# Kernel tuning notes

Hardware: AMD Instinct MI355X
Metric: run time of the kernel (lower is better)

## Reference

```python
import jax, jax.numpy as jnp
import numpy as np

# Model dims
C = 16          # in_channels / d_model
D_INNER = 64    # expand * C, expand = 64 // C = 4
HEADDIM = 4
NHEADS = D_INNER // HEADDIM   # 16
D_STATE = 64
D_CONV = 4
CONV_DIM = D_INNER + 2 * D_STATE        # 192 (x, B, C streams)
D_IN_PROJ = 2 * D_INNER + 2 * D_STATE + NHEADS  # 272 (z, xBC, dt)
# Input volume
BSZ, DD, HH, WW = 8, 32, 16, 16
L = DD * HH * WW  # 8192, multiple of 256 -> exact adaptive max pool
POOL = 256


def setup_inputs():
    key = jax.random.key(0)
    ks = jax.random.split(key, 10)
    x = jax.random.normal(ks[0], (BSZ, C, DD, HH, WW), jnp.float32)
    # 3 independent Mamba2 blocks -> stack params with leading dim 3
    Win = jax.random.normal(ks[1], (3, D_IN_PROJ, C), jnp.float32) / np.sqrt(C).astype(np.float32)
    conv_w = jax.random.normal(ks[2], (3, CONV_DIM, D_CONV), jnp.float32) / np.sqrt(D_CONV).astype(np.float32)
    conv_b = jax.random.normal(ks[3], (3, CONV_DIM), jnp.float32) * 0.1
    dt_bias = jax.random.normal(ks[4], (3, NHEADS), jnp.float32) * 0.5
    A_log = jnp.log(jax.random.uniform(ks[5], (3, NHEADS), jnp.float32, minval=1.0, maxval=16.0))
    Dp = jax.random.normal(ks[6], (3, NHEADS), jnp.float32) * 0.5 + 1.0
    norm_w = jnp.ones((3, D_INNER), jnp.float32)
    Wout = jax.random.normal(ks[7], (3, C, D_INNER), jnp.float32) / np.sqrt(D_INNER).astype(np.float32)
    gamma = jnp.ones((3, C), jnp.float32)
    beta = jnp.zeros((3, C), jnp.float32)
    lin_w = jax.random.normal(ks[8], (3, 1, C), jnp.float32) / np.sqrt(C).astype(np.float32)
    lin_b = jnp.zeros((3, 1), jnp.float32)
    return dict(x=x, Win=Win, conv_w=conv_w, conv_b=conv_b, dt_bias=dt_bias,
                A_log=A_log, Dp=Dp, norm_w=norm_w, Wout=Wout,
                gamma=gamma, beta=beta, lin_w=lin_w, lin_b=lin_b)


def _mamba2(u, Win, conv_w, conv_b, dt_bias, A_log, Dp, norm_w, Wout):
    """Mamba2 block: u (B, L, C) -> (B, L, C). ngroups=1, rmsnorm gated."""
    B, Lx, _ = u.shape
    zxbcdt = jnp.einsum('blc,pc->blp', u, Win)  # (B, L, 272)
    z = zxbcdt[..., :D_INNER]
    xBC = zxbcdt[..., D_INNER:D_INNER + CONV_DIM]
    dt = jax.nn.softplus(zxbcdt[..., D_INNER + CONV_DIM:] + dt_bias)  # (B, L, H)
    # causal depthwise conv over time
    conv = jax.lax.conv_general_dilated(
        jnp.transpose(xBC, (0, 2, 1)), conv_w[:, None, :], (1,),
        [(D_CONV - 1, 0)], feature_group_count=CONV_DIM)
    xBC = jax.nn.silu(jnp.transpose(conv, (0, 2, 1)) + conv_b)
    xh = xBC[..., :D_INNER].reshape(B, Lx, NHEADS, HEADDIM)
    Bm = xBC[..., D_INNER:D_INNER + D_STATE]   # (B, L, N)
    Cm = xBC[..., D_INNER + D_STATE:]          # (B, L, N)
    A = -jnp.exp(A_log)                        # (H,)
    dA = jnp.exp(dt * A)                       # (B, L, H)
    dtx = dt[..., None] * xh                   # (B, L, H, P)

    def step(S, inp):
        dA_t, dtx_t, B_t, C_t = inp
        S = S * dA_t[:, :, None, None] + dtx_t[..., None] * B_t[:, None, None, :]
        y_t = jnp.einsum('bhpn,bn->bhp', S, C_t)
        return S, y_t

    S0 = jnp.zeros((B, NHEADS, HEADDIM, D_STATE), u.dtype)
    xs = (jnp.moveaxis(dA, 1, 0), jnp.moveaxis(dtx, 1, 0),
          jnp.moveaxis(Bm, 1, 0), jnp.moveaxis(Cm, 1, 0))
    _, ys = jax.lax.scan(step, S0, xs)                       # (L, B, H, P)
    y = jnp.moveaxis(ys, 0, 1) + Dp[None, None, :, None] * xh
    y = y.reshape(B, Lx, D_INNER) * jax.nn.silu(z)           # gate first
    y = y * jax.lax.rsqrt(jnp.mean(y * y, -1, keepdims=True) + 1e-5) * norm_w
    return jnp.einsum('bld,cd->blc', y, Wout)


def _proj_pool(y, gamma, beta, lw, lb):
    """ReLU -> BatchNorm1d (batch stats) -> Linear(C,1) -> AdaptiveMaxPool1d(256)."""
    B, Lx, _ = y.shape
    v = jax.nn.relu(y.reshape(-1, C))
    mu = jnp.mean(v, 0)
    var = jnp.mean((v - mu) ** 2, 0)
    v = (v - mu) * jax.lax.rsqrt(var + 1e-5) * gamma + beta
    s = (v @ lw.T + lb).reshape(B, Lx)
    return jnp.max(s.reshape(B, POOL, Lx // POOL), -1)  # (B, 256)


def reference(x, Win, conv_w, conv_b, dt_bias, A_log, Dp, norm_w, Wout,
              gamma, beta, lin_w, lin_b):
    B, Cc, Dd, Hh, Ww = x.shape
    Lx = Dd * Hh * Ww
    fD = jnp.transpose(x.reshape(B, Cc, Lx), (0, 2, 1))
    fH = jnp.transpose(jnp.transpose(x, (0, 1, 3, 4, 2)).reshape(B, Cc, Lx), (0, 2, 1))
    fW = jnp.transpose(jnp.transpose(x, (0, 1, 4, 2, 3)).reshape(B, Cc, Lx), (0, 2, 1))
    seqs = jnp.stack([fD, fH, fW], 0)  # (3, B, L, C)
    ys = jax.vmap(_mamba2)(seqs, Win, conv_w, conv_b, dt_bias, A_log, Dp, norm_w, Wout)
    pooled = jax.vmap(_proj_pool)(ys, gamma, beta, lin_w, lin_b)  # (3, B, 256)
    return jnp.concatenate([pooled[0], pooled[1], pooled[2]], -1)[:, None, :]  # (B,1,768)
```

## Files before the change

kernel.cpp:

```cpp
#include <hip/hip_runtime.h>
#include <math.h>

#define CONVD 192
#define NC 128
#define PW 32
#define LOG2E 1.4426950408889634f
#define LN2f  0.69314718055994531f

#define OFF_DST   0u
#define OFF_CHA   4194304u
#define OFF_YS    4210688u
#define OFF_PART  5259264u
#define OFF_TILE  5267456u
#define PD        19947520u

#define TXH 0
#define TC  4096
#define TG  8192
#define TDT 12288
#define TCT 13312

#define XSW(m, t)   ((m) * 64 + (((((t) >> 2) ^ ((m) & 15)) & 15) << 2) + ((t) & 3))
#define XSW4(m, tq) ((m) * 64 + ((((tq) ^ ((m) & 15)) & 15) << 2))

typedef float f32x2 __attribute__((ext_vector_type(2)));

__device__ __forceinline__ f32x2 pk_fma(f32x2 a, f32x2 b, f32x2 c) {
    f32x2 d;
    asm("v_pk_fma_f32 %0, %1, %2, %3" : "=v"(d) : "v"(a), "v"(b), "v"(c));
    return d;
}
__device__ __forceinline__ f32x2 lo2(float4 v) { f32x2 r; r.x = v.x; r.y = v.y; return r; }
__device__ __forceinline__ f32x2 hi2(float4 v) { f32x2 r; r.x = v.z; r.y = v.w; return r; }

__device__ __forceinline__ float fast_silu(float x) {
    float e = __builtin_amdgcn_exp2f(-x * LOG2E);
    return x * __builtin_amdgcn_rcpf(1.f + e);
}
__device__ __forceinline__ float fast_softplus(float x) {
    if (x > 20.f) return x;
    float e = __builtin_amdgcn_exp2f(x * LOG2E);
    return LN2f * __builtin_amdgcn_logf(1.f + e);
}

template<int NT>
__device__ __forceinline__ void stage_u(
    const float* __restrict__ x, float* u_s, int b, int l0, int dir, int tid)
{
    for (int i = tid; i < 67 * 16; i += NT) {
        int pos = i >> 4, c = i & 15;
        int l = l0 + pos - 3;
        float v = 0.f;
        if (l >= 0) {
            if (dir == 0) {
                v = x[(b * 16 + c) * 8192 + l];
            } else if (dir == 1) {
                int h = l >> 9, w = (l >> 5) & 15, d = l & 31;
                v = x[(((b * 16 + c) * 32 + d) * 16 + h) * 16 + w];
            } else {
                int w = l >> 9, d = (l >> 4) & 31, h = l & 15;
                v = x[(((b * 16 + c) * 32 + d) * 16 + h) * 16 + w];
            }
        }
        u_s[pos * 17 + c] = v;
    }
}

__device__ __forceinline__ float pk_dot16(const f32x2* u2, const float* wp) {
    float4 w0 = *(const float4*)(wp);
    float4 w1 = *(const float4*)(wp + 4);
    float4 w2 = *(const float4*)(wp + 8);
    float4 w3 = *(const float4*)(wp + 12);
    f32x2 a = {0.f, 0.f};
    a = pk_fma(u2[0], lo2(w0), a);
    a = pk_fma(u2[1], hi2(w0), a);
    a = pk_fma(u2[2], lo2(w1), a);
    a = pk_fma(u2[3], hi2(w1), a);
    a = pk_fma(u2[4], lo2(w2), a);
    a = pk_fma(u2[5], hi2(w2), a);
    a = pk_fma(u2[6], lo2(w3), a);
    a = pk_fma(u2[7], hi2(w3), a);
    return a.x + a.y;
}

__global__ __launch_bounds__(512, 6) void k_front(
    const float* __restrict__ x, const float* __restrict__ Win,
    const float* __restrict__ convw, const float* __restrict__ convb,
    const float* __restrict__ dtb, const float* __restrict__ A_log,
    float* __restrict__ ws, int dir0, int dslm)
{
    __shared__ float u_s[67 * 17];
    __shared__ float xh_c[4096];
    __shared__ float Bs[4096];
    __shared__ float dts[16 * 65];
    __shared__ float wbuf[16 * 65];
    const int tid = threadIdx.x;
    const int ck = blockIdx.x;
    const int b = blockIdx.y;
    const int dir = dir0 + blockIdx.z;
    float* base = ws + (size_t)(dslm * blockIdx.z) * PD;
    float* Dst = base + OFF_DST;
    float* chA = base + OFF_CHA;
    float* tile = base + OFF_TILE + (size_t)(b * 128 + ck) * 14336;
    const int l0 = ck * 64;
    float* halo = wbuf;

    stage_u<512>(x, u_s, b, l0, dir, tid);
    __syncthreads();

    const int lane = tid & 63;
    const int wv = __builtin_amdgcn_readfirstlane(tid >> 6);

    f32x2 u2[8];
    {
        const float* ur = &u_s[(lane + 3) * 17];
        #pragma unroll
        for (int k = 0; k < 8; k++) { u2[k].x = ur[2 * k]; u2[k].y = ur[2 * k + 1]; }
    }
    if (tid < 192) {
        f32x2 uh2[8];
        #pragma unroll
        for (int pos = 0; pos < 3; pos++) {
            const float* uhr = &u_s[pos * 17];
            #pragma unroll
            for (int k = 0; k < 8; k++) { uh2[k].x = uhr[2 * k]; uh2[k].y = uhr[2 * k + 1]; }
            halo[pos * 192 + tid] = pk_dot16(uh2, Win + (size_t)(dir * 272 + 64 + tid) * 16);
        }
    }
    __syncthreads();

    for (int i = 0; i < 26; i++) {
        const int col = 64 + wv * 26 + i;
        float acc = pk_dot16(u2, Win + (size_t)(dir * 272 + col) * 16);
        if (col < 256) {
            const int ch = col - 64;
            float v1 = __shfl_up(acc, 1);
            float v2 = __shfl_up(acc, 2);
            float v3 = __shfl_up(acc, 3);
            float hh0 = halo[ch];
            float hh1 = halo[192 + ch];
            float hh2 = halo[384 + ch];
            float m1 = (lane >= 1) ? v1 : hh2;
            float m2 = (lane >= 2) ? v2 : ((lane == 0) ? hh1 : hh2);
            float m3 = (lane >= 3) ? v3 : ((lane == 0) ? hh0 : ((lane == 1) ? hh1 : hh2));
            const float* cwp = convw + (size_t)(dir * CONVD + ch) * 4;
            float conv = convb[dir * CONVD + ch]
                       + cwp[0] * m3 + cwp[1] * m2 + cwp[2] * m1 + cwp[3] * acc;
            float xv = fast_silu(conv);
            if (ch < 64)       xh_c[XSW(ch, lane)] = xv;
            else if (ch < 128) Bs[XSW(ch - 64, lane)] = xv;
            else               tile[TC + (ch - 128) * 64 + lane] = xv;
        } else {
            const int h = col - 256;
            float dv = fast_softplus(acc + dtb[dir * 16 + h]);
            dts[h * 65 + lane] = dv;
            tile[TDT + h * 64 + lane] = dv;
        }
    }
    __syncthreads();

    for (int j4 = tid; j4 < 1024; j4 += 512) {
        ((float4*)(tile + TXH))[j4] = ((const float4*)xh_c)[j4];
    }
    for (int h = wv; h < 16; h += 8) {
        float A2 = -expf(A_log[dir * 16 + h]) * LOG2E;
        float dtv = dts[h * 65 + lane];
        float v = dtv * A2;
        #pragma unroll
        for (int off = 1; off < 64; off <<= 1) {
            float o = __shfl_up(v, off, 64);
            if (lane >= off) v += o;
        }
        float tot = __shfl(v, 63, 64);
        tile[TCT + h * 64 + lane] = v;
        wbuf[h * 65 + lane] = __builtin_amdgcn_exp2f(tot - v) * dtv;
        if (lane == 63) chA[(b * 16 + h) * 128 + ck] = __builtin_amdgcn_exp2f(tot);
    }
    __syncthreads();

    for (int j = tid; j < 4096; j += 512) {
        int hp = j >> 6, t = j & 63;
        xh_c[XSW(hp, t)] *= wbuf[(hp >> 2) * 65 + t];
    }
    __syncthreads();

    if (tid < 256) {
        const int hp4 = tid >> 4, n4 = tid & 15;
        f32x2 a2[4][4] = {};
        for (int tq = 0; tq < 16; tq++) {
            float4 xv[4], bv[4];
            #pragma unroll
            for (int i2 = 0; i2 < 4; i2++) {
                xv[i2] = *(const float4*)&xh_c[XSW4(4 * hp4 + i2, tq)];
                bv[i2] = *(const float4*)&Bs[XSW4(4 * n4 + i2, tq)];
            }
            #pragma unroll
            for (int i2 = 0; i2 < 4; i2++)
                #pragma unroll
                for (int j2 = 0; j2 < 4; j2++) {
                    a2[i2][j2] = pk_fma(lo2(xv[i2]), lo2(bv[j2]), a2[i2][j2]);
                    a2[i2][j2] = pk_fma(hi2(xv[i2]), hi2(bv[j2]), a2[i2][j2]);
                }
        }
        #pragma unroll
        for (int i2 = 0; i2 < 4; i2++) {
            int hp = 4 * hp4 + i2;
            int h = hp >> 2, p = hp & 3;
            *(float4*)(Dst + ((size_t)((b * 16 + h) * 128 + ck)) * 256 + p * 64 + 4 * n4) =
                make_float4(a2[i2][0].x + a2[i2][0].y, a2[i2][1].x + a2[i2][1].y,
                            a2[i2][2].x + a2[i2][2].y, a2[i2][3].x + a2[i2][3].y);
        }
    } else {
        const int tg2 = tid - 256;
        const int t4g = tg2 >> 4, x4g = tg2 & 15;
        float G_[4][4] = {};
        for (int n = 0; n < 64; n++) {
            float4 cr4 = *(const float4*)(tile + TC + n * 64 + 4 * t4g);
            float4 br4 = *(const float4*)&Bs[XSW4(n, x4g)];
            float cr[4] = {cr4.x, cr4.y, cr4.z, cr4.w};
            float br_[4] = {br4.x, br4.y, br4.z, br4.w};
            #pragma unroll
            for (int r = 0; r < 4; r++)
                #pragma unroll
                for (int q = 0; q < 4; q++)
                    G_[r][q] += cr[r] * br_[q];
        }
        float* gdst = tile + TG + (size_t)tg2 * 16;
        #pragma unroll
        for (int r = 0; r < 4; r++)
            *(float4*)(gdst + 4 * r) = make_float4(G_[r][0], G_[r][1], G_[r][2], G_[r][3]);
    }
}

__global__ __launch_bounds__(64) void k_chunk_scan(
    float* __restrict__ ws, int dslm)
{
    float* base = ws + (size_t)(dslm * blockIdx.z) * PD;
    float* Dst = base + OFF_DST;
    const float* chA = base + OFF_CHA;
    const int bh = blockIdx.x >> 2;
    const int elem = (blockIdx.x & 3) * 64 + threadIdx.x;
    float S = 0.f;
    for (int k0 = 0; k0 < NC; k0 += 8) {
        float d[8], av[8];
        #pragma unroll
        for (int j = 0; j < 8; j++) {
            d[j] = Dst[((size_t)(bh * 128 + k0 + j)) * 256 + elem];
            av[j] = chA[bh * 128 + k0 + j];
        }
        #pragma unroll
        for (int j = 0; j < 8; j++) {
            Dst[((size_t)(bh * 128 + k0 + j)) * 256 + elem] = S;
            S = av[j] * S + d[j];
        }
    }
}

__global__ __launch_bounds__(512, 2) void k_out_epi(
    const float* __restrict__ x, const float* __restrict__ Win,
    const float* __restrict__ Dp, const float* __restrict__ normw,
    const float* __restrict__ Wout, float* __restrict__ ws, int dir0, int dslm)
{
    __shared__ float SinT[64 * 68];
    __shared__ float xh_c[4096];
    __shared__ float Bz[4096];
    __shared__ float Cy[4352];
    __shared__ float uW[67 * 17];
    __shared__ float dts[16 * 68];
    __shared__ float ct2l[16 * 68];
    __shared__ float Dps[16];
    float* base = ws + (size_t)(dslm * blockIdx.z) * PD;
    const float* Dst = base + OFF_DST;
    float* ys        = base + OFF_YS;
    float* partials  = base + OFF_PART;
    const float* tile = base + OFF_TILE + (size_t)(blockIdx.y * 128 + blockIdx.x) * 14336;
    const int dir = dir0 + blockIdx.z;
    const int tid = threadIdx.x;
    const int b = blockIdx.y;
    const int ck = blockIdx.x;
    const int l0 = ck * 64;
    const int tg = tid & 255;
    const int t4 = tg >> 4, x4 = tg & 15;
    const int grp = tid >> 8;
    const int lane = tid & 63;
    const int wv = __builtin_amdgcn_readfirstlane(tid >> 6);

    stage_u<512>(x, uW, b, l0, dir, tid);
    for (int j4 = tid; j4 < 1024; j4 += 512) {
        ((float4*)xh_c)[j4] = ((const float4*)(tile + TXH))[j4];
        ((float4*)Cy)[j4]   = ((const float4*)(tile + TC))[j4];
    }
    if (tid < 256) {
        int h = tid >> 4, tq = tid & 15;
        *(float4*)&dts[h * 68 + 4 * tq]  = ((const float4*)(tile + TDT))[tid];
        *(float4*)&ct2l[h * 68 + 4 * tq] = ((const float4*)(tile + TCT))[tid];
    }
    for (int j = tid; j < 1024; j += 512) {
        int hp = j >> 4, n4 = (j & 15) << 2;
        int h = hp >> 2, p = hp & 3;
        float4 sv = *(const float4*)(Dst + ((size_t)((b * 16 + h) * 128 + ck)) * 256 + p * 64 + n4);
        SinT[(n4 + 0) * 68 + hp] = sv.x;
        SinT[(n4 + 1) * 68 + hp] = sv.y;
        SinT[(n4 + 2) * 68 + hp] = sv.z;
        SinT[(n4 + 3) * 68 + hp] = sv.w;
    }
    float G_[4][4];
    {
        const float* gsrc = tile + TG + (size_t)tg * 16;
        #pragma unroll
        for (int r = 0; r < 4; r++) {
            float4 g4 = *(const float4*)(gsrc + 4 * r);
            G_[r][0] = g4.x; G_[r][1] = g4.y; G_[r][2] = g4.z; G_[r][3] = g4.w;
        }
    }
    if (tid < 16) Dps[tid] = Dp[dir * 16 + tid];
    __syncthreads();

    {
        f32x2 u2[8];
        const float* ur = &uW[(lane + 3) * 17];
        #pragma unroll
        for (int k = 0; k < 8; k++) { u2[k].x = ur[2 * k]; u2[k].y = ur[2 * k + 1]; }
        for (int i = 0; i < 8; i++) {
            const int col = wv * 8 + i;
            Bz[XSW(col, lane)] = pk_dot16(u2, Win + (size_t)(dir * 272 + col) * 16);
        }
    }
    float CS_[4][4] = {};
    {
        const int n0 = grp << 5;
        for (int n = n0; n < n0 + 32; n++) {
            float4 cr4 = *(const float4*)&Cy[n * 64 + 4 * t4];
            float cr[4] = {cr4.x, cr4.y, cr4.z, cr4.w};
            float sn[4];
            #pragma unroll
            for (int q = 0; q < 4; q++) sn[q] = SinT[n * 68 + 4 * x4 + q];
            #pragma unroll
            for (int r = 0; r < 4; r++)
                #pragma unroll
                for (int q = 0; q < 4; q++)
                    CS_[r][q] += cr[r] * sn[q];
        }
    }
    __syncthreads();

    {
        float* ex = (grp == 0) ? SinT : Cy;
        #pragma unroll
        for (int k = 0; k < 16; k++) ex[tg * 17 + k] = CS_[k >> 2][k & 3];
    }
    for (int j = tid; j < 1024; j += 512) {
        int c = j >> 6, d = j & 63;
        uW[c * 65 + d] = Wout[dir * 1024 + j] * normw[dir * 64 + d];
    }
    __syncthreads();
    {
        const float* ex = (grp == 0) ? Cy : SinT;
        #pragma unroll
        for (int k = 0; k < 16; k++) CS_[k >> 2][k & 3] += ex[tg * 17 + k];
    }
    __syncthreads();

    float* yv = Cy;
    const int tbase = 4 * t4;
    #pragma unroll 1
    for (int hh = 0; hh < 8; hh++) {
        const int h = 8 * grp + hh;
        const float* ctp = &ct2l[h * 68];
        const float* dtp = &dts[h * 68];
        float4 ctt4 = *(const float4*)&ctp[tbase];
        const float ctt[4] = {ctt4.x, ctt4.y, ctt4.z, ctt4.w};
        float ect[4];
        #pragma unroll
        for (int r = 0; r < 4; r++) ect[r] = __builtin_amdgcn_exp2f(ctt[r]);
        float4 cs4 = *(const float4*)&ctp[4 * x4];
        float4 dt4 = *(const float4*)&dtp[4 * x4];
        float v[16] = {0.f, 0.f, 0.f, 0.f, 0.f, 0.f, 0.f, 0.f,
                       0.f, 0.f, 0.f, 0.f, 0.f, 0.f, 0.f, 0.f};
        #pragma unroll
        for (int q = 0; q < 4; q++) {
            const int s = 4 * x4 + q;
            float csq = (q == 0) ? cs4.x : (q == 1) ? cs4.y : (q == 2) ? cs4.z : cs4.w;
            float dtq = (q == 0) ? dt4.x : (q == 1) ? dt4.y : (q == 2) ? dt4.z : dt4.w;
            float xv[4];
            #pragma unroll
            for (int p = 0; p < 4; p++) {
                int m = 4 * h + p;
                xv[p] = xh_c[m * 64 + (((x4 ^ (m & 15)) & 15) << 2) + q];
            }
            #pragma unroll
            for (int r = 0; r < 4; r++) {
                float e = __builtin_amdgcn_exp2f(ctt[r] - csq);
                float w = (s <= tbase + r) ? (G_[r][q] * dtq) * e : 0.f;
                #pragma unroll
                for (int p = 0; p < 4; p++) v[4 * r + p] += w * xv[p];
            }
        }
        if (x4 == h) {
            #pragma unroll
            for (int r = 0; r < 4; r++)
                #pragma unroll
                for (int p = 0; p < 4; p++)
                    v[4 * r + p] += ect[r] * CS_[r][p];
        }
        #pragma unroll
        for (int j = 0; j < 8; j++) {
            float a = (x4 & 8) ? v[j + 8] : v[j];
            float s_ = (x4 & 8) ? v[j] : v[j + 8];
            v[j] = a + __shfl_xor(s_, 8);
        }
        #pragma unroll
        for (int j = 0; j < 4; j++) {
            float a = (x4 & 4) ? v[j + 4] : v[j];
            float s_ = (x4 & 4) ? v[j] : v[j + 4];
            v[j] = a + __shfl_xor(s_, 4);
        }
        #pragma unroll
        for (int j = 0; j < 2; j++) {
            float a = (x4 & 2) ? v[j + 2] : v[j];
            float s_ = (x4 & 2) ? v[j] : v[j + 2];
            v[j] = a + __shfl_xor(s_, 2);
        }
        {
            float a = (x4 & 1) ? v[1] : v[0];
            float s_ = (x4 & 1) ? v[0] : v[1];
            v[0] = a + __shfl_xor(s_, 1);
        }
        const int row = tbase + (x4 >> 2);
        yv[(row * 4 + (x4 & 3)) * 17 + h] = v[0];
    }
    __syncthreads();

    float* red = ct2l;
    float os[4];
    const int row = tid >> 2;
    const int p = tid & 3;
    if (tid < 256) {
        float gg[16], sumsq = 0.f;
        #pragma unroll
        for (int h = 0; h < 16; h++) {
            float yval = yv[(row * 4 + p) * 17 + h];
            int m = 4 * h + p;
            int ax = m * 64 + ((((row >> 2) ^ (m & 15)) & 15) << 2) + (row & 3);
            float xh = xh_c[ax];
            float zv = Bz[ax];
            float val = (yval + Dps[h] * xh) * fast_silu(zv);
            gg[h] = val;
            sumsq += val * val;
        }
        sumsq += __shfl_xor(sumsq, 1);
        sumsq += __shfl_xor(sumsq, 2);
        float rms = rsqrtf(sumsq * (1.f / 64.f) + 1e-5f);

        float oc[16];
        #pragma unroll
        for (int c = 0; c < 16; c++) {
            float a = 0.f;
            #pragma unroll
            for (int h = 0; h < 16; h++) a += gg[h] * uW[c * 65 + 4 * h + p];
            oc[c] = a;
        }
        #pragma unroll
        for (int c = 0; c < 16; c++) {
            oc[c] += __shfl_xor(oc[c], 1);
            oc[c] += __shfl_xor(oc[c], 2);
        }
        #pragma unroll
        for (int i2 = 0; i2 < 4; i2++) {
            float a0 = (p == 0) ? oc[i2] : oc[4 + i2];
            float a1 = (p == 2) ? oc[8 + i2] : oc[12 + i2];
            os[i2] = (((p & 2) == 0) ? a0 : a1) * rms;
        }
        size_t bl = (size_t)(b * 8192 + l0 + row);
        *(float4*)(ys + bl * 16 + 4 * p) = make_float4(os[0], os[1], os[2], os[3]);

        float bs[4], bq[4];
        #pragma unroll
        for (int i2 = 0; i2 < 4; i2++) {
            float vv = fmaxf(os[i2], 0.f);
            bs[i2] = vv;
            bq[i2] = vv * vv;
        }
        #pragma unroll
        for (int off = 4; off < 64; off <<= 1) {
            #pragma unroll
            for (int i2 = 0; i2 < 4; i2++) {
                bs[i2] += __shfl_xor(bs[i2], off);
                bq[i2] += __shfl_xor(bq[i2], off);
            }
        }
        const int wlane = tid & 63, wvid = tid >> 6;
        if (wlane < 4) {
            #pragma unroll
            for (int i2 = 0; i2 < 4; i2++) {
                red[wvid * 34 + 4 * wlane + i2] = bs[i2];
                red[wvid * 34 + 16 + 4 * wlane + i2] = bq[i2];
            }
        }
    }
    __syncthreads();
    if (tid < 32) {
        float a = red[0 * 34 + tid] + red[1 * 34 + tid]
                + red[2 * 34 + tid] + red[3 * 34 + tid];
        partials[((size_t)(b * 128 + ck)) * 32 + tid] = a;
    }
}

__global__ __launch_bounds__(256) void k_pool_bn(
    const float* __restrict__ gamma, const float* __restrict__ beta,
    const float* __restrict__ lin_w, const float* __restrict__ lin_b,
    float* __restrict__ ws, float* __restrict__ out, int dir0, int dslm)
{
    float* base = ws + (size_t)(dslm * blockIdx.z) * PD;
    const float* ys = base + OFF_YS;
    const float* partials = base + OFF_PART;
    const int dir = dir0 + blockIdx.z;
    const int tid = threadIdx.x;
    __shared__ float red[8][33];
    __shared__ float cf[18];
    {
        int c = tid & 31, ks = tid >> 5;
        float a = 0.f;
        for (int k = ks * 128; k < ks * 128 + 128; k++) a += partials[k * 32 + c];
        red[ks][c] = a;
    }
    __syncthreads();
    if (tid < 32) {
        float a = 0.f;
        #pragma unroll
        for (int s2 = 1; s2 < 8; s2++) a += red[s2][tid];
        red[0][tid] += a;
    }
    __syncthreads();
    if (tid == 0) {
        float off = lin_b[dir];
        for (int c = 0; c < 16; c++) {
            float mu = red[0][c] * (1.f / 65536.f);
            float var = red[0][16 + c] * (1.f / 65536.f) - mu * mu;
            float inv = rsqrtf(var + 1e-5f);
            float coef = inv * gamma[dir * 16 + c] * lin_w[dir * 16 + c];
            cf[c] = coef;
            off += beta[dir * 16 + c] * lin_w[dir * 16 + c] - mu * coef;
        }
        cf[16] = off;
    }
    __syncthreads();

    const int b = blockIdx.x >> 3;
    const int jg = blockIdx.x & 7;
    const int j = jg * 32 + (tid >> 3);
    const int sub = tid & 7;
    float m = -3.4e38f;
    #pragma unroll
    for (int r = 0; r < 4; r++) {
        int l = j * PW + 8 * r + sub;
        const float* rowp = ys + (size_t)(b * 8192 + l) * 16;
        float sv = cf[16];
        #pragma unroll
        for (int k = 0; k < 4; k++) {
            float4 v4 = *(const float4*)(rowp + 4 * k);
            sv += fmaxf(v4.x, 0.f) * cf[4 * k] + fmaxf(v4.y, 0.f) * cf[4 * k + 1]
                + fmaxf(v4.z, 0.f) * cf[4 * k + 2] + fmaxf(v4.w, 0.f) * cf[4 * k + 3];
        }
        m = fmaxf(m, sv);
    }
    m = fmaxf(m, __shfl_xor(m, 1));
    m = fmaxf(m, __shfl_xor(m, 2));
    m = fmaxf(m, __shfl_xor(m, 4));
    if (sub == 0) out[b * 768 + dir * 256 + j] = m;
}

extern "C" void kernel_launch(void* const* d_in, const int* in_sizes, int n_in,
                              void* d_out, int out_size, void* d_ws, size_t ws_size,
                              hipStream_t stream) {
    const float* x     = (const float*)d_in[0];
    const float* Win   = (const float*)d_in[1];
    const float* convw = (const float*)d_in[2];
    const float* convb = (const float*)d_in[3];
    const float* dtb   = (const float*)d_in[4];
    const float* Alog  = (const float*)d_in[5];
    const float* Dp    = (const float*)d_in[6];
    const float* normw = (const float*)d_in[7];
    const float* Wout  = (const float*)d_in[8];
    const float* gamma = (const float*)d_in[9];
    const float* beta  = (const float*)d_in[10];
    const float* linw  = (const float*)d_in[11];
    const float* linb  = (const float*)d_in[12];
    float* out = (float*)d_out;
    float* ws = (float*)d_ws;

    const bool batched = ws_size >= (size_t)3 * PD * 4;
    const int nz = batched ? 3 : 1;
    const int dslm = batched ? 1 : 0;
    const int nloop = batched ? 1 : 3;

    for (int d0 = 0; d0 < nloop; ++d0) {
        k_front<<<dim3(128, 8, nz), dim3(512), 0, stream>>>(
            x, Win, convw, convb, dtb, Alog, ws, d0, dslm);
        k_chunk_scan<<<dim3(512, 1, nz), dim3(64), 0, stream>>>(ws, dslm);
        k_out_epi<<<dim3(128, 8, nz), dim3(512), 0, stream>>>(
            x, Win, Dp, normw, Wout, ws, d0, dslm);
        k_pool_bn<<<dim3(64, 1, nz), dim3(256), 0, stream>>>(
            gamma, beta, linw, linb, ws, out, d0, dslm);
    }
}
```

Measured before the change: 368.3 us.

## Recompute x and C streams in output kernel instead of round-tripping workspace

k_front no longer writes the post-conv x and C tiles to the global workspace. k_out_epi now recomputes the in-projection, the causal conv with its halo, and SiLU for the x and C channels from the staged input. This shrinks the per-chunk tile and the overall workspace, removing a large global write and read between kernels. The cost is extra projection and conv arithmetic plus more barriers in k_out_epi. k_front also gains a shared C buffer, and its launch-bounds occupancy hint drops from 6 to 4. Some leftover dead code remains in the new halo setup.

```diff
diff --git a/kernel.cpp b/kernel.cpp
--- a/kernel.cpp
+++ b/kernel.cpp
@@ -12,13 +12,11 @@
 #define OFF_YS    4210688u
 #define OFF_PART  5259264u
 #define OFF_TILE  5267456u
-#define PD        19947520u
-
-#define TXH 0
-#define TC  4096
-#define TG  8192
-#define TDT 12288
-#define TCT 13312
+#define PD        11558912u
+
+#define TG  0
+#define TDT 4096
+#define TCT 5120
 
 #define XSW(m, t)   ((m) * 64 + (((((t) >> 2) ^ ((m) & 15)) & 15) << 2) + ((t) & 3))
 #define XSW4(m, tq) ((m) * 64 + ((((tq) ^ ((m) & 15)) & 15) << 2))
@@ -83,7 +81,7 @@
     return a.x + a.y;
 }
 
-__global__ __launch_bounds__(512, 6) void k_front(
+__global__ __launch_bounds__(512, 4) void k_front(
     const float* __restrict__ x, const float* __restrict__ Win,
     const float* __restrict__ convw, const float* __restrict__ convb,
     const float* __restrict__ dtb, const float* __restrict__ A_log,
@@ -92,6 +90,7 @@
     __shared__ float u_s[67 * 17];
     __shared__ float xh_c[4096];
     __shared__ float Bs[4096];
+    __shared__ float Cc[4096];
     __shared__ float dts[16 * 65];
     __shared__ float wbuf[16 * 65];
     const int tid = threadIdx.x;
@@ -101,7 +100,7 @@
     float* base = ws + (size_t)(dslm * blockIdx.z) * PD;
     float* Dst = base + OFF_DST;
     float* chA = base + OFF_CHA;
-    float* tile = base + OFF_TILE + (size_t)(b * 128 + ck) * 14336;
+    float* tile = base + OFF_TILE + (size_t)(b * 128 + ck) * 6144;
     const int l0 = ck * 64;
     float* halo = wbuf;
 
@@ -149,7 +148,7 @@
             float xv = fast_silu(conv);
             if (ch < 64)       xh_c[XSW(ch, lane)] = xv;
             else if (ch < 128) Bs[XSW(ch - 64, lane)] = xv;
-            else               tile[TC + (ch - 128) * 64 + lane] = xv;
+            else               Cc[XSW(ch - 128, lane)] = xv;
         } else {
             const int h = col - 256;
             float dv = fast_softplus(acc + dtb[dir * 16 + h]);
@@ -159,9 +158,6 @@
     }
     __syncthreads();
 
-    for (int j4 = tid; j4 < 1024; j4 += 512) {
-        ((float4*)(tile + TXH))[j4] = ((const float4*)xh_c)[j4];
-    }
     for (int h = wv; h < 16; h += 8) {
         float A2 = -expf(A_log[dir * 16 + h]) * LOG2E;
         float dtv = dts[h * 65 + lane];
@@ -215,7 +211,7 @@
         const int t4g = tg2 >> 4, x4g = tg2 & 15;
         float G_[4][4] = {};
         for (int n = 0; n < 64; n++) {
-            float4 cr4 = *(const float4*)(tile + TC + n * 64 + 4 * t4g);
+            float4 cr4 = *(const float4*)&Cc[XSW4(n, t4g)];
             float4 br4 = *(const float4*)&Bs[XSW4(n, x4g)];
             float cr[4] = {cr4.x, cr4.y, cr4.z, cr4.w};
             float br_[4] = {br4.x, br4.y, br4.z, br4.w};
@@ -258,6 +254,7 @@
 
 __global__ __launch_bounds__(512, 2) void k_out_epi(
     const float* __restrict__ x, const float* __restrict__ Win,
+    const float* __restrict__ convw, const float* __restrict__ convb,
     const float* __restrict__ Dp, const float* __restrict__ normw,
     const float* __restrict__ Wout, float* __restrict__ ws, int dir0, int dslm)
 {
@@ -273,7 +270,7 @@
     const float* Dst = base + OFF_DST;
     float* ys        = base + OFF_YS;
     float* partials  = base + OFF_PART;
-    const float* tile = base + OFF_TILE + (size_t)(blockIdx.y * 128 + blockIdx.x) * 14336;
+    const float* tile = base + OFF_TILE + (size_t)(blockIdx.y * 128 + blockIdx.x) * 6144;
     const int dir = dir0 + blockIdx.z;
     const int tid = threadIdx.x;
     const int b = blockIdx.y;
@@ -286,10 +283,6 @@
     const int wv = __builtin_amdgcn_readfirstlane(tid >> 6);
 
     stage_u<512>(x, uW, b, l0, dir, tid);
-    for (int j4 = tid; j4 < 1024; j4 += 512) {
-        ((float4*)xh_c)[j4] = ((const float4*)(tile + TXH))[j4];
-        ((float4*)Cy)[j4]   = ((const float4*)(tile + TC))[j4];
-    }
     if (tid < 256) {
         int h = tid >> 4, tq = tid & 15;
         *(float4*)&dts[h * 68 + 4 * tq]  = ((const float4*)(tile + TDT))[tid];
@@ -304,33 +297,82 @@
         SinT[(n4 + 2) * 68 + hp] = sv.z;
         SinT[(n4 + 3) * 68 + hp] = sv.w;
     }
-    float G_[4][4];
+    if (tid < 16) Dps[tid] = Dp[dir * 16 + tid];
+    __syncthreads();
+
+    f32x2 u2[8];
     {
-        const float* gsrc = tile + TG + (size_t)tg * 16;
-        #pragma unroll
-        for (int r = 0; r < 4; r++) {
-            float4 g4 = *(const float4*)(gsrc + 4 * r);
-            G_[r][0] = g4.x; G_[r][1] = g4.y; G_[r][2] = g4.z; G_[r][3] = g4.w;
-        }
-    }
-    if (tid < 16) Dps[tid] = Dp[dir * 16 + tid];
-    __syncthreads();
-
-    {
-        f32x2 u2[8];
         const float* ur = &uW[(lane + 3) * 17];
         #pragma unroll
         for (int k = 0; k < 8; k++) { u2[k].x = ur[2 * k]; u2[k].y = ur[2 * k + 1]; }
-        for (int i = 0; i < 8; i++) {
-            const int col = wv * 8 + i;
-            Bz[XSW(col, lane)] = pk_dot16(u2, Win + (size_t)(dir * 272 + col) * 16);
-        }
-    }
+    }
+    f32x2 uh2[8];
+    if (tid < 192) {
+        #pragma unroll
+        for (int k = 0; k < 8; k++) { uh2[k].x = uW[2 * k]; uh2[k].y = uW[2 * k + 1]; }
+        #pragma unroll
+        for (int k = 0; k < 8; k++) {
+            uh2[k].x = 0.f;
+        }
+    }
+    __syncthreads();
+    float* halo = uW;
+    if (tid < 192) {
+        #pragma unroll
+        for (int pos = 0; pos < 3; pos++) {
+            (void)0;
+        }
+    }
+    f32x2 uh0[8], uh1[8], uh2b[8];
+    if (tid < 192) {
+        #pragma unroll
+        for (int k = 0; k < 8; k++) {
+            uh0[k].x = uW[0 * 17 + 2 * k];  uh0[k].y = uW[0 * 17 + 2 * k + 1];
+            uh1[k].x = uW[1 * 17 + 2 * k];  uh1[k].y = uW[1 * 17 + 2 * k + 1];
+            uh2b[k].x = uW[2 * 17 + 2 * k]; uh2b[k].y = uW[2 * 17 + 2 * k + 1];
+        }
+    }
+    __syncthreads();
+    if (tid < 192) {
+        const float* wp = Win + (size_t)(dir * 272 + 64 + tid) * 16;
+        halo[0 * 192 + tid] = pk_dot16(uh0, wp);
+        halo[1 * 192 + tid] = pk_dot16(uh1, wp);
+        halo[2 * 192 + tid] = pk_dot16(uh2b, wp);
+    }
+    __syncthreads();
+
+    for (int i = 0; i < 24; i++) {
+        const int j = wv * 24 + i;
+        const int pcol = (j < 128) ? j : (j + 64);
+        float acc = pk_dot16(u2, Win + (size_t)(dir * 272 + pcol) * 16);
+        if (pcol < 64) {
+            Bz[XSW(pcol, lane)] = acc;
+        } else {
+            const int ch = pcol - 64;
+            float v1 = __shfl_up(acc, 1);
+            float v2 = __shfl_up(acc, 2);
+            float v3 = __shfl_up(acc, 3);
+            float hh0 = halo[ch];
+            float hh1 = halo[192 + ch];
+            float hh2 = halo[384 + ch];
+            float m1 = (lane >= 1) ? v1 : hh2;
+            float m2 = (lane >= 2) ? v2 : ((lane == 0) ? hh1 : hh2);
+            float m3 = (lane >= 3) ? v3 : ((lane == 0) ? hh0 : ((lane == 1) ? hh1 : hh2));
+            const float* cwp = convw + (size_t)(dir * CONVD + ch) * 4;
+            float conv = convb[dir * CONVD + ch]
+                       + cwp[0] * m3 + cwp[1] * m2 + cwp[2] * m1 + cwp[3] * acc;
+            float xv = fast_silu(conv);
+            if (ch < 64) xh_c[XSW(ch, lane)] = xv;
+            else         Cy[XSW(ch - 128, lane)] = xv;
+        }
+    }
+    __syncthreads();
+
     float CS_[4][4] = {};
     {
         const int n0 = grp << 5;
         for (int n = n0; n < n0 + 32; n++) {
-            float4 cr4 = *(const float4*)&Cy[n * 64 + 4 * t4];
+            float4 cr4 = *(const float4*)&Cy[XSW4(n, t4)];
             float cr[4] = {cr4.x, cr4.y, cr4.z, cr4.w};
             float sn[4];
             #pragma unroll
@@ -358,6 +400,15 @@
         const float* ex = (grp == 0) ? Cy : SinT;
         #pragma unroll
         for (int k = 0; k < 16; k++) CS_[k >> 2][k & 3] += ex[tg * 17 + k];
+    }
+    float G_[4][4];
+    {
+        const float* gsrc = tile + TG + (size_t)tg * 16;
+        #pragma unroll
+        for (int r = 0; r < 4; r++) {
+            float4 g4 = *(const float4*)(gsrc + 4 * r);
+            G_[r][0] = g4.x; G_[r][1] = g4.y; G_[r][2] = g4.z; G_[r][3] = g4.w;
+        }
     }
     __syncthreads();
 
@@ -599,7 +650,7 @@
             x, Win, convw, convb, dtb, Alog, ws, d0, dslm);
         k_chunk_scan<<<dim3(512, 1, nz), dim3(64), 0, stream>>>(ws, dslm);
         k_out_epi<<<dim3(128, 8, nz), dim3(512), 0, stream>>>(
-            x, Win, Dp, normw, Wout, ws, d0, dslm);
+            x, Win, convw, convb, Dp, normw, Wout, ws, d0, dslm);
         k_pool_bn<<<dim3(64, 1, nz), dim3(256), 0, stream>>>(
             gamma, beta, linw, linb, ws, out, d0, dslm);
     }
```

Measured after the change: 481.9 us. +30.8%, slower.
